# Performance work log

Hardware: AMD Instinct MI355X
Metric: run time of the kernel (lower is better)

Reference implementation:

```python
import jax, jax.numpy as jnp
import numpy as np

EMBED_DIM = 1024
NUM_HEADS = 16
HEAD_DIM = EMBED_DIM // NUM_HEADS  # 64
B, NQ, NK = 4, 1024, 2048


def setup_inputs() -> dict:
    key = jax.random.key(0)
    ks = jax.random.split(key, 13)
    s = 1.0 / np.sqrt(EMBED_DIM)
    inp = {
        "query": jax.random.normal(ks[0], (B, NQ, EMBED_DIM), jnp.float32),
        "key": jax.random.normal(ks[1], (B, NK, EMBED_DIM), jnp.float32),
        "value": jax.random.normal(ks[2], (B, NK, EMBED_DIM), jnp.float32),
        # positive multiplicity weights per key element
        "key_multiplicities": jax.random.uniform(ks[3], (B, NK), jnp.float32, 0.1, 4.0),
        "wq_w": jax.random.normal(ks[4], (EMBED_DIM, EMBED_DIM), jnp.float32) * s,
        "wq_b": jnp.zeros((EMBED_DIM,), jnp.float32),
        "wk_w": jax.random.normal(ks[5], (EMBED_DIM, EMBED_DIM), jnp.float32) * s,
        "wk_b": jnp.zeros((EMBED_DIM,), jnp.float32),
        "wv_w": jax.random.normal(ks[6], (EMBED_DIM, EMBED_DIM), jnp.float32) * s,
        "wv_b": jnp.zeros((EMBED_DIM,), jnp.float32),
        "wo_w": jax.random.normal(ks[7], (EMBED_DIM, EMBED_DIM), jnp.float32) * s,
        "wo_b": jnp.zeros((EMBED_DIM,), jnp.float32),
    }
    return inp


def _split_heads(x, b, n):
    # (b, n, h*d) -> (b, h, n, d)
    return x.reshape(b, n, NUM_HEADS, HEAD_DIM).transpose(0, 2, 1, 3)


def reference(query, key, value, key_multiplicities,
              wq_w, wq_b, wk_w, wk_b, wv_w, wv_b, wo_w, wo_b):
    b, n_q, _ = query.shape
    _, n_k, _ = key.shape
    q = _split_heads(query @ wq_w.T + wq_b, b, n_q)   # (b, h, n_q, d)
    k = _split_heads(key @ wk_w.T + wk_b, b, n_k)     # (b, h, n_k, d)
    v = _split_heads(value @ wv_w.T + wv_b, b, n_k)   # (b, h, n_k, d)
    scale = 1.0 / jnp.sqrt(jnp.asarray(HEAD_DIM, q.dtype))
    scores = jnp.einsum("bhqd,bhkd->bhqk", q, k) * scale
    # multiplicities weight each key: softmax_i(m_i * exp(s_i)) == softmax(s_i + log m_i)
    logits = scores + jnp.log(key_multiplicities)[:, None, None, :]
    attn = jax.nn.softmax(logits, axis=-1)            # (b, h, n_q, n_k)
    out = jnp.einsum("bhqk,bhkd->bhqd", attn, v)
    out = out.transpose(0, 2, 1, 3).reshape(b, n_q, NUM_HEADS * HEAD_DIM)
    return out @ wo_w.T + wo_b
```

## Files before the change

### kernel.cpp

```cpp
#include <hip/hip_runtime.h>
#include <hip/hip_bf16.h>
#include <stdint.h>
#include <stddef.h>

typedef __attribute__((ext_vector_type(8))) short bf16x8;
typedef __attribute__((ext_vector_type(4))) short short4v;
typedef __attribute__((ext_vector_type(4))) float f32x4;
typedef __attribute__((ext_vector_type(2))) uint32_t u32x2;
typedef __attribute__((ext_vector_type(4))) uint32_t u32x4;

#define MFMA16(a, b, c) __builtin_amdgcn_mfma_f32_16x16x32_bf16((a), (b), (c), 0, 0, 0)

__device__ __forceinline__ short f2bf(float f) {
    uint32_t u = __builtin_bit_cast(uint32_t, f);
    u = (u + 0x7FFFu + ((u >> 16) & 1u)) >> 16;
    return (short)(uint16_t)u;
}

__device__ __forceinline__ uint32_t pkbf(float a, float b) {
#if __has_builtin(__builtin_amdgcn_cvt_pk_bf16_f32)
    auto r = __builtin_amdgcn_cvt_pk_bf16_f32(a, b);
    return __builtin_bit_cast(uint32_t, r);
#else
    return (uint32_t)(uint16_t)f2bf(a) | ((uint32_t)(uint16_t)f2bf(b) << 16);
#endif
}

__device__ __forceinline__ float fexp2(float x) {
#if __has_builtin(__builtin_amdgcn_exp2f)
    return __builtin_amdgcn_exp2f(x);
#else
    return exp2f(x);
#endif
}

__device__ __forceinline__ void gload16(const short* g, short* l) {
    __builtin_amdgcn_global_load_lds(
        (const __attribute__((address_space(1))) unsigned int*)g,
        (__attribute__((address_space(3))) unsigned int*)l, 16, 0, 0);
}

__global__ __launch_bounds__(256) void prep_kernel(
        const float* __restrict__ w0, const float* __restrict__ w1,
        const float* __restrict__ w2, const float* __restrict__ w3,
        const float* __restrict__ m, short* __restrict__ wb,
        float* __restrict__ lm) {
    const int bid = blockIdx.x;
    if (bid >= 2048) {
        const int i = ((bid - 2048) * 256 + threadIdx.x) * 8;
        f32x4 a = *(const f32x4*)(m + i);
        f32x4 b = *(const f32x4*)(m + i + 4);
        f32x4 oa, ob;
        #pragma unroll
        for (int j = 0; j < 4; ++j) { oa[j] = __log2f(a[j]); ob[j] = __log2f(b[j]); }
        *(f32x4*)(lm + i) = oa;
        *(f32x4*)(lm + i + 4) = ob;
        return;
    }
    const int z = bid >> 9;
    const int local = bid & 511;
    const float* src = (z == 0) ? w0 : (z == 1) ? w1 : (z == 2) ? w2 : w3;
    short* dst = wb + (size_t)z * 1048576;
    const size_t i = ((size_t)local * 256 + threadIdx.x) * 8;
    f32x4 a = *(const f32x4*)(src + i);
    f32x4 b = *(const f32x4*)(src + i + 4);
    u32x4 o = { pkbf(a[0], a[1]), pkbf(a[2], a[3]), pkbf(b[0], b[1]), pkbf(b[2], b[3]) };
    *(u32x4*)(dst + i) = o;
}

__global__ __launch_bounds__(256) void proj_kernel(
        const float* __restrict__ Qf, const float* __restrict__ Kf,
        const float* __restrict__ Vf, const short* __restrict__ wb,
        const float* __restrict__ wq_b, const float* __restrict__ wk_b,
        const float* __restrict__ wv_b, short* __restrict__ Qp,
        short* __restrict__ Kp, short* __restrict__ Vt) {
    __shared__ short As[4][4096];
    __shared__ short Bs[4][4096];

    const int cpx = gridDim.x >> 3;
    const int l = (blockIdx.x & 7) * cpx + (blockIdx.x >> 3);
    const int y = l >> 3;
    const int tn = (l & 7) * 128;

    const float* A; const short* W; const float* bias; int mode, tm;
    if (y < 32)      { A = Qf; W = wb;           bias = wq_b; mode = 0; tm = y * 128; }
    else if (y < 96) { A = Kf; W = wb + 1048576; bias = wk_b; mode = 1; tm = (y - 32) * 128; }
    else             { A = Vf; W = wb + 2097152; bias = wv_b; mode = 2; tm = (y - 96) * 128; }

    const int t = threadIdx.x, lane = t & 63, w = t >> 6;
    const int wr = w >> 1, wc = w & 1;
    const int qd = lane >> 4, c = lane & 15;

    f32x4 acc[4][4];
    #pragma unroll
    for (int i = 0; i < 4; ++i)
        #pragma unroll
        for (int j = 0; j < 4; ++j) acc[i][j] = (f32x4){0.f, 0.f, 0.f, 0.f};

    const int r0 = w * 16 + (lane >> 2);
    const int qc = (lane & 3) ^ ((lane >> 3) & 3);
    const float* gaf0 = A + (size_t)(tm + r0) * 1024 + qc * 8;
    const float* gaf1 = gaf0 + 64 * 1024;
    const short* gb0 = W + (size_t)(tn + r0) * 1024 + qc * 8;
    const short* gb1 = gb0 + 64 * 1024;
    const int lofs = w * 512;
    const int swz = (qd ^ ((c >> 1) & 3)) * 8;

    for (int k0 = 0; k0 < 1024; k0 += 128) {
        __syncthreads();
        #pragma unroll
        for (int kh = 0; kh < 4; ++kh) {
            gload16(gb0 + k0 + kh * 32, &Bs[kh][lofs]);
            gload16(gb1 + k0 + kh * 32, &Bs[kh][lofs + 2048]);
        }
        #pragma unroll
        for (int kh = 0; kh < 4; ++kh) {
            f32x4 a0 = *(const f32x4*)(gaf0 + k0 + kh * 32);
            f32x4 a1 = *(const f32x4*)(gaf0 + k0 + kh * 32 + 4);
            f32x4 b0 = *(const f32x4*)(gaf1 + k0 + kh * 32);
            f32x4 b1 = *(const f32x4*)(gaf1 + k0 + kh * 32 + 4);
            u32x4 pa = { pkbf(a0[0], a0[1]), pkbf(a0[2], a0[3]),
                         pkbf(a1[0], a1[1]), pkbf(a1[2], a1[3]) };
            u32x4 pb = { pkbf(b0[0], b0[1]), pkbf(b0[2], b0[3]),
                         pkbf(b1[0], b1[1]), pkbf(b1[2], b1[3]) };
            *(u32x4*)&As[kh][lofs + lane * 8]        = pa;
            *(u32x4*)&As[kh][lofs + 2048 + lane * 8] = pb;
        }
        __syncthreads();
        #pragma unroll
        for (int kh = 0; kh < 4; ++kh) {
            bf16x8 af[4], bfr[4];
            #pragma unroll
            for (int rt = 0; rt < 4; ++rt)
                af[rt] = *(const bf16x8*)&As[kh][(wr * 64 + rt * 16 + c) * 32 + swz];
            #pragma unroll
            for (int ct = 0; ct < 4; ++ct)
                bfr[ct] = *(const bf16x8*)&Bs[kh][(wc * 64 + ct * 16 + c) * 32 + swz];
            #pragma unroll
            for (int rt = 0; rt < 4; ++rt)
                #pragma unroll
                for (int ct = 0; ct < 4; ++ct)
                    acc[rt][ct] = MFMA16(af[rt], bfr[ct], acc[rt][ct]);
        }
    }

    float bv[4];
    #pragma unroll
    for (int ct = 0; ct < 4; ++ct) bv[ct] = bias[tn + wc * 64 + ct * 16 + c];

    if (mode == 2) {
        #pragma unroll
        for (int rt = 0; rt < 4; ++rt)
            #pragma unroll
            for (int ct = 0; ct < 4; ++ct) {
                const int cg = tn + wc * 64 + ct * 16 + c;
                const int h = cg >> 6, d = cg & 63;
                const int rg0 = tm + wr * 64 + rt * 16 + qd * 4;
                const int bb = rg0 >> 11, n = rg0 & 2047;
                u32x2 pk = { pkbf(acc[rt][ct][0] + bv[ct], acc[rt][ct][1] + bv[ct]),
                             pkbf(acc[rt][ct][2] + bv[ct], acc[rt][ct][3] + bv[ct]) };
                *(u32x2*)&Vt[((((size_t)(bb * 16 + h)) * 64 + d) << 11) + n] = pk;
            }
    } else {
        short* out = (mode == 0) ? Qp : Kp;
        const int nshift = (mode == 0) ? 10 : 11;
        const int mask = (1 << nshift) - 1;
        #pragma unroll
        for (int rt = 0; rt < 4; ++rt)
            #pragma unroll
            for (int ct = 0; ct < 4; ++ct) {
                const int cg = tn + wc * 64 + ct * 16 + c;
                const int h = cg >> 6, d = cg & 63;
                #pragma unroll
                for (int r = 0; r < 4; ++r) {
                    const int rg = tm + wr * 64 + rt * 16 + qd * 4 + r;
                    const int bb = rg >> nshift, n = rg & mask;
                    out[((((size_t)(bb * 16 + h)) << nshift) + n) * 64 + d] =
                        f2bf(acc[rt][ct][r] + bv[ct]);
                }
            }
    }
}

__global__ __launch_bounds__(256, 4) void gemm_o_kernel(
        const short* __restrict__ Ob, const short* __restrict__ W,
        const float* __restrict__ bias, float* __restrict__ out) {
    __shared__ short As[4][128 * 32];
    __shared__ short Bs[4][64 * 32];

    const int cpx = gridDim.x >> 3;
    const int l = (blockIdx.x & 7) * cpx + (blockIdx.x >> 3);
    const int tm = (l >> 4) * 128, tn = (l & 15) * 64;

    const int t = threadIdx.x, lane = t & 63, w = t >> 6;
    const int wr = w >> 1, wc = w & 1;
    const int qd = lane >> 4, c = lane & 15;

    f32x4 acc[4][2];
    #pragma unroll
    for (int i = 0; i < 4; ++i)
        #pragma unroll
        for (int j = 0; j < 2; ++j) acc[i][j] = (f32x4){0.f, 0.f, 0.f, 0.f};

    const int r0 = w * 16 + (lane >> 2);
    const int qc = (lane & 3) ^ ((lane >> 3) & 3);
    const short* ga0 = Ob + (size_t)(tm + r0) * 1024 + qc * 8;
    const short* ga1 = ga0 + 64 * 1024;
    const short* gb0 = W + (size_t)(tn + r0) * 1024 + qc * 8;
    const int lofs = w * 512;
    const int swz = (qd ^ ((c >> 1) & 3)) * 8;

    for (int k0 = 0; k0 < 1024; k0 += 128) {
        __syncthreads();
        #pragma unroll
        for (int kh = 0; kh < 4; ++kh) {
            gload16(ga0 + k0 + kh * 32, &As[kh][lofs]);
            gload16(ga1 + k0 + kh * 32, &As[kh][lofs + 2048]);
            gload16(gb0 + k0 + kh * 32, &Bs[kh][lofs]);
        }
        __syncthreads();
        #pragma unroll
        for (int kh = 0; kh < 4; ++kh) {
            bf16x8 af[4], bfr[2];
            #pragma unroll
            for (int rt = 0; rt < 4; ++rt)
                af[rt] = *(const bf16x8*)&As[kh][(wr * 64 + rt * 16 + c) * 32 + swz];
            #pragma unroll
            for (int ct = 0; ct < 2; ++ct)
                bfr[ct] = *(const bf16x8*)&Bs[kh][(wc * 32 + ct * 16 + c) * 32 + swz];
            #pragma unroll
            for (int rt = 0; rt < 4; ++rt)
                #pragma unroll
                for (int ct = 0; ct < 2; ++ct)
                    acc[rt][ct] = MFMA16(af[rt], bfr[ct], acc[rt][ct]);
        }
    }

    float bv[2];
    #pragma unroll
    for (int ct = 0; ct < 2; ++ct) bv[ct] = bias[tn + wc * 32 + ct * 16 + c];

    #pragma unroll
    for (int rt = 0; rt < 4; ++rt)
        #pragma unroll
        for (int ct = 0; ct < 2; ++ct) {
            const int cg = tn + wc * 32 + ct * 16 + c;
            #pragma unroll
            for (int r = 0; r < 4; ++r) {
                const int rg = tm + wr * 64 + rt * 16 + qd * 4 + r;
                out[(size_t)rg * 1024 + cg] = acc[rt][ct][r] + bv[ct];
            }
        }
}

__global__ __launch_bounds__(256, 2) void attn_kernel(
        const short* __restrict__ Qp, const short* __restrict__ Kp,
        const short* __restrict__ Vt, const float* __restrict__ logm,
        short* __restrict__ Ob) {
    __shared__ short Ps[128 * 128];
    __shared__ short Vs[64 * 128];
    __shared__ float Lm[128];
    short* Ks = Ps;

    const int bid = blockIdx.x;
    const int xcd = bid & 7, ii = bid >> 3;
    const int qt = ii >> 3, bh = xcd + ((ii & 7) << 3);
    const int b = bh >> 4;
    const int t = threadIdx.x, lane = t & 63, w = t >> 6;
    const int qd = lane >> 4, c = lane & 15;
    const int cl = c & 7;
    const float SC = 0.18033688011112042f;

    bf16x8 qf[2][2];
    #pragma unroll
    for (int ct = 0; ct < 2; ++ct)
        #pragma unroll
        for (int kd = 0; kd < 2; ++kd)
            qf[ct][kd] = *(const bf16x8*)(Qp +
                ((size_t)bh * 1024 + qt * 128 + w * 32 + ct * 16 + c) * 64 + kd * 32 + qd * 8);

    bf16x8 onesf;
    {
        const short ov = (c == 0) ? (short)0x3F80 : (short)0;
        #pragma unroll
        for (int j = 0; j < 8; ++j) onesf[j] = ov;
    }

    f32x4 oacc[2][5];
    #pragma unroll
    for (int i = 0; i < 2; ++i)
        #pragma unroll
        for (int j = 0; j < 5; ++j) oacc[i][j] = (f32x4){0.f, 0.f, 0.f, 0.f};

    const short* kgp[4];
    short* klp[4];
    const short* vgp[4];
    short* vlp[4];
    {
        const int krow = lane >> 3;
        const int kchk = (lane & 7) ^ krow;
        const int vrow = lane >> 4;
        #pragma unroll
        for (int i = 0; i < 4; ++i) {
            const int rk = w * 32 + i * 8 + krow;
            kgp[i] = Kp + ((size_t)bh * 2048 + rk) * 64 + kchk * 8;
            klp[i] = &Ks[(w * 4 + i) * 512];
            const int rv = w * 16 + i * 4 + vrow;
            const int vchk = (lane & 15) ^ (rv & 7);
            vgp[i] = Vt + ((size_t)bh * 64 + rv) * 2048 + vchk * 8;
            vlp[i] = &Vs[(w * 4 + i) * 512];
        }
    }

    for (int kt = 0; kt < 16; ++kt) {
        #pragma unroll
        for (int i = 0; i < 4; ++i) {
            gload16(kgp[i] + (size_t)kt * 8192, klp[i]);
            gload16(vgp[i] + kt * 128, vlp[i]);
        }
        if (t < 128) Lm[t] = logm[b * 2048 + kt * 128 + t];
        __syncthreads();

        f32x4 s[8][2];
        #pragma unroll
        for (int rt = 0; rt < 8; ++rt) {
            bf16x8 a0 = *(const bf16x8*)&Ks[(rt * 16 + c) * 64 + (qd ^ cl) * 8];
            bf16x8 a1 = *(const bf16x8*)&Ks[(rt * 16 + c) * 64 + ((4 | qd) ^ cl) * 8];
            #pragma unroll
            for (int ct = 0; ct < 2; ++ct) {
                f32x4 z = (f32x4){0.f, 0.f, 0.f, 0.f};
                s[rt][ct] = MFMA16(a1, qf[ct][1], MFMA16(a0, qf[ct][0], z));
            }
        }
        __syncthreads();

        #pragma unroll
        for (int rt = 0; rt < 8; ++rt) {
            f32x4 lv = *(const f32x4*)&Lm[rt * 16 + qd * 4];
            #pragma unroll
            for (int ct = 0; ct < 2; ++ct) {
                float p0 = fexp2(__builtin_fmaf(s[rt][ct][0], SC, lv[0]));
                float p1 = fexp2(__builtin_fmaf(s[rt][ct][1], SC, lv[1]));
                float p2 = fexp2(__builtin_fmaf(s[rt][ct][2], SC, lv[2]));
                float p3 = fexp2(__builtin_fmaf(s[rt][ct][3], SC, lv[3]));
                u32x2 pk = { pkbf(p0, p1), pkbf(p2, p3) };
                const int prow = w * 32 + ct * 16 + c;
                const int pch = (2 * rt + (qd >> 1)) ^ cl;
                *(u32x2*)&Ps[prow * 128 + pch * 8 + (qd & 1) * 4] = pk;
            }
        }

        #pragma unroll
        for (int kk = 0; kk < 4; ++kk) {
            const int lch = ((kk * 4 + qd) ^ cl) * 8;
            bf16x8 pf[2], vf[4];
            #pragma unroll
            for (int rtq = 0; rtq < 2; ++rtq)
                pf[rtq] = *(const bf16x8*)&Ps[(w * 32 + rtq * 16 + c) * 128 + lch];
            #pragma unroll
            for (int ct = 0; ct < 4; ++ct)
                vf[ct] = *(const bf16x8*)&Vs[(ct * 16 + c) * 128 + lch];
            #pragma unroll
            for (int rtq = 0; rtq < 2; ++rtq) {
                #pragma unroll
                for (int ct = 0; ct < 4; ++ct)
                    oacc[rtq][ct] = MFMA16(pf[rtq], vf[ct], oacc[rtq][ct]);
                oacc[rtq][4] = MFMA16(pf[rtq], onesf, oacc[rtq][4]);
            }
        }
        __syncthreads();
    }

    const int h = bh & 15;
    float inv[2][4];
    #pragma unroll
    for (int rtq = 0; rtq < 2; ++rtq)
        #pragma unroll
        for (int r = 0; r < 4; ++r)
            inv[rtq][r] = 1.f / __shfl(oacc[rtq][4][r], qd * 16);
    #pragma unroll
    for (int rtq = 0; rtq < 2; ++rtq)
        #pragma unroll
        for (int ct = 0; ct < 4; ++ct)
            #pragma unroll
            for (int r = 0; r < 4; ++r) {
                const int qg = qt * 128 + w * 32 + rtq * 16 + qd * 4 + r;
                const int e = h * 64 + ct * 16 + c;
                Ob[((size_t)(b * 1024 + qg)) * 1024 + e] = f2bf(oacc[rtq][ct][r] * inv[rtq][r]);
            }
}

extern "C" void kernel_launch(void* const* d_in, const int* in_sizes, int n_in,
                              void* d_out, int out_size, void* d_ws, size_t ws_size,
                              hipStream_t stream) {
    (void)in_sizes; (void)n_in; (void)out_size; (void)ws_size;
    const float* query = (const float*)d_in[0];
    const float* key   = (const float*)d_in[1];
    const float* value = (const float*)d_in[2];
    const float* mult  = (const float*)d_in[3];
    const float* wq_w  = (const float*)d_in[4];
    const float* wq_b  = (const float*)d_in[5];
    const float* wk_w  = (const float*)d_in[6];
    const float* wk_b  = (const float*)d_in[7];
    const float* wv_w  = (const float*)d_in[8];
    const float* wv_b  = (const float*)d_in[9];
    const float* wo_w  = (const float*)d_in[10];
    const float* wo_b  = (const float*)d_in[11];
    float* out = (float*)d_out;

    char* ws = (char*)d_ws;
    const size_t MB = 1024 * 1024;
    short* wb = (short*)(ws + 0 * MB);
    short* Qp = (short*)(ws + 8 * MB);
    short* Kp = (short*)(ws + 16 * MB);
    short* Vt = (short*)(ws + 32 * MB);
    short* Ob = (short*)(ws + 48 * MB);
    float* lm = (float*)(ws + 56 * MB);

    prep_kernel<<<dim3(2052), 256, 0, stream>>>(
        wq_w, wk_w, wv_w, wo_w, mult, wb, lm);
    proj_kernel<<<dim3(1280), 256, 0, stream>>>(
        query, key, value, wb, wq_b, wk_b, wv_b, Qp, Kp, Vt);
    attn_kernel<<<dim3(512), 256, 0, stream>>>(Qp, Kp, Vt, lm, Ob);
    gemm_o_kernel<<<dim3(512), 256, 0, stream>>>(Ob, wb + 3145728, wo_b, out);
}
```

Before: 293.4 us.

## Load fp32 activations directly into LDS and convert to bf16 at fragment read

The projection GEMM now stages the fp32 A tile into shared memory with global_load_lds, using an XOR swizzle, instead of loading it through registers, converting and storing bf16. The bf16 conversion moves to fragment read time. The K-step shrinks from 128 to 64 to fit the doubled fp32 LDS footprint. This removes register round-trips and VALU stores in the load phase, but doubles the number of barriers and k-iterations and repeats the conversion for each wave that reads the same data.

Result: slower. 320.2 us (+9.1%).

```diff
diff --git a/kernel.cpp b/kernel.cpp
--- a/kernel.cpp
+++ b/kernel.cpp
@@ -35,6 +35,11 @@
 }
 
 __device__ __forceinline__ void gload16(const short* g, short* l) {
+    __builtin_amdgcn_global_load_lds(
+        (const __attribute__((address_space(1))) unsigned int*)g,
+        (__attribute__((address_space(3))) unsigned int*)l, 16, 0, 0);
+}
+__device__ __forceinline__ void gload16f(const float* g, float* l) {
     __builtin_amdgcn_global_load_lds(
         (const __attribute__((address_space(1))) unsigned int*)g,
         (__attribute__((address_space(3))) unsigned int*)l, 16, 0, 0);
@@ -74,8 +79,8 @@
         const float* __restrict__ wq_b, const float* __restrict__ wk_b,
         const float* __restrict__ wv_b, short* __restrict__ Qp,
         short* __restrict__ Kp, short* __restrict__ Vt) {
-    __shared__ short As[4][4096];
-    __shared__ short Bs[4][4096];
+    __shared__ __align__(16) float Af[2][4096];
+    __shared__ __align__(16) short Bs[2][4096];
 
     const int cpx = gridDim.x >> 3;
     const int l = (blockIdx.x & 7) * cpx + (blockIdx.x >> 3);
@@ -90,6 +95,7 @@
     const int t = threadIdx.x, lane = t & 63, w = t >> 6;
     const int wr = w >> 1, wc = w & 1;
     const int qd = lane >> 4, c = lane & 15;
+    const int cx = c & 7;
 
     f32x4 acc[4][4];
     #pragma unroll
@@ -99,40 +105,39 @@
 
     const int r0 = w * 16 + (lane >> 2);
     const int qc = (lane & 3) ^ ((lane >> 3) & 3);
-    const float* gaf0 = A + (size_t)(tm + r0) * 1024 + qc * 8;
-    const float* gaf1 = gaf0 + 64 * 1024;
     const short* gb0 = W + (size_t)(tn + r0) * 1024 + qc * 8;
     const short* gb1 = gb0 + 64 * 1024;
     const int lofs = w * 512;
     const int swz = (qd ^ ((c >> 1) & 3)) * 8;
 
-    for (int k0 = 0; k0 < 1024; k0 += 128) {
-        __syncthreads();
-        #pragma unroll
-        for (int kh = 0; kh < 4; ++kh) {
+    const int arow = lane >> 3;
+    const int acol = ((lane & 7) ^ arow) * 4;
+    const float* gA = A + (size_t)(tm + w * 32 + arow) * 1024 + acol;
+    const int lAo = w * 1024;
+
+    for (int k0 = 0; k0 < 1024; k0 += 64) {
+        __syncthreads();
+        #pragma unroll
+        for (int kh = 0; kh < 2; ++kh) {
             gload16(gb0 + k0 + kh * 32, &Bs[kh][lofs]);
             gload16(gb1 + k0 + kh * 32, &Bs[kh][lofs + 2048]);
-        }
-        #pragma unroll
-        for (int kh = 0; kh < 4; ++kh) {
-            f32x4 a0 = *(const f32x4*)(gaf0 + k0 + kh * 32);
-            f32x4 a1 = *(const f32x4*)(gaf0 + k0 + kh * 32 + 4);
-            f32x4 b0 = *(const f32x4*)(gaf1 + k0 + kh * 32);
-            f32x4 b1 = *(const f32x4*)(gaf1 + k0 + kh * 32 + 4);
-            u32x4 pa = { pkbf(a0[0], a0[1]), pkbf(a0[2], a0[3]),
-                         pkbf(a1[0], a1[1]), pkbf(a1[2], a1[3]) };
-            u32x4 pb = { pkbf(b0[0], b0[1]), pkbf(b0[2], b0[3]),
-                         pkbf(b1[0], b1[1]), pkbf(b1[2], b1[3]) };
-            *(u32x4*)&As[kh][lofs + lane * 8]        = pa;
-            *(u32x4*)&As[kh][lofs + 2048 + lane * 8] = pb;
-        }
-        __syncthreads();
-        #pragma unroll
-        for (int kh = 0; kh < 4; ++kh) {
+            #pragma unroll
+            for (int g = 0; g < 4; ++g)
+                gload16f(gA + (size_t)g * 8192 + k0 + kh * 32, &Af[kh][lAo + g * 256]);
+        }
+        __syncthreads();
+        #pragma unroll
+        for (int kh = 0; kh < 2; ++kh) {
             bf16x8 af[4], bfr[4];
             #pragma unroll
-            for (int rt = 0; rt < 4; ++rt)
-                af[rt] = *(const bf16x8*)&As[kh][(wr * 64 + rt * 16 + c) * 32 + swz];
+            for (int rt = 0; rt < 4; ++rt) {
+                const int ab = (wr * 64 + rt * 16 + c) * 32;
+                f32x4 lo = *(const f32x4*)&Af[kh][ab + (((qd << 1)    ) ^ cx) * 4];
+                f32x4 hi = *(const f32x4*)&Af[kh][ab + (((qd << 1) | 1) ^ cx) * 4];
+                u32x4 fr = { pkbf(lo[0], lo[1]), pkbf(lo[2], lo[3]),
+                             pkbf(hi[0], hi[1]), pkbf(hi[2], hi[3]) };
+                af[rt] = __builtin_bit_cast(bf16x8, fr);
+            }
             #pragma unroll
             for (int ct = 0; ct < 4; ++ct)
                 bfr[ct] = *(const bf16x8*)&Bs[kh][(wc * 64 + ct * 16 + c) * 32 + swz];
```
